# Optimization experiments

Hardware: AMD Instinct MI355X
Metric: run time of the kernel (lower is better)

Reference implementation:

```python
import jax, jax.numpy as jnp
import numpy as np

B, T, IN, CELL, OUT = 512, 32, 512, 128, 128


def setup_inputs() -> dict:
    key = jax.random.key(0)
    ks = jax.random.split(key, 6)
    d = IN + CELL
    w = lambda k, shape, fan: jax.random.normal(k, shape, jnp.float32) / np.sqrt(fan).astype(np.float32)
    return {
        "x": jax.random.normal(ks[0], (B, T, IN), jnp.float32),
        "Wf": w(ks[1], (d, CELL), d), "bf": jnp.zeros((CELL,), jnp.float32),
        "Wi1": w(ks[2], (d, CELL), d), "bi1": jnp.zeros((CELL,), jnp.float32),
        "Wi2": w(ks[3], (d, CELL), d), "bi2": jnp.zeros((CELL,), jnp.float32),
        "Wo": w(ks[4], (d, CELL), d), "bo": jnp.zeros((CELL,), jnp.float32),
        "Wc": w(ks[5], (CELL, OUT), CELL), "bc": jnp.zeros((OUT,), jnp.float32),
    }


def reference(x, Wf, bf, Wi1, bi1, Wi2, bi2, Wo, bo, Wc, bc):
    # Faithful to MyLSTM.forward: loop runs x.shape[1] times; each iteration
    # concatenates the FULL [B,T,CELL] cell_state with the FULL [B,T,IN] x
    # (x is never sliced per step). Only the last iteration's output matters,
    # but we carry it through the scan to match the loop structure exactly.
    Tn = x.shape[1]
    c0 = jnp.zeros(x.shape[:2] + (Wf.shape[1],), x.dtype)
    out0 = jnp.zeros(x.shape[:2] + (Wc.shape[1],), x.dtype)

    def step(carry, _):
        c, _prev_out = carry
        inp = jnp.concatenate([c, x], axis=-1)  # [B,T,CELL+IN]
        f = jax.nn.sigmoid(inp @ Wf + bf)
        c = c * f + jax.nn.sigmoid(inp @ Wi1 + bi1) * jnp.tanh(inp @ Wi2 + bi2)
        o = jax.nn.sigmoid(inp @ Wo + bo) * jnp.tanh(c)
        out = jax.nn.softmax(o @ Wc + bc, axis=2)  # out_features != 1 branch
        return (c, out), None

    (c, out), _ = jax.lax.scan(step, (c0, out0), None, length=Tn)
    return out, c
```

## Files before the change

kernel.cpp:

```cpp
#include <hip/hip_runtime.h>
#include <stdint.h>

#define ROWS  16384
#define CELL  128
#define INF   512
#define RPB   16
#define NSTEP 32

typedef _Float16 f16x8 __attribute__((ext_vector_type(8)));
typedef _Float16 f16x4 __attribute__((ext_vector_type(4)));
typedef float    f32x4 __attribute__((ext_vector_type(4)));

#define MFMA16(a, b, c) __builtin_amdgcn_mfma_f32_16x16x32_f16((a), (b), (c), 0, 0, 0)

#define AOFF  0
#define XOFF  65536
#define WCOFF 327680
#define WSTOT 344064

#define LOG2E  1.44269504f
#define LOG2E2 2.88539008f

__device__ __forceinline__ unsigned short f2h_bits(float f) {
  _Float16 h = (_Float16)f;
  return *(unsigned short*)&h;
}
__device__ __forceinline__ float sig2(float z) {
  return __builtin_amdgcn_rcpf(1.f + __builtin_amdgcn_exp2f(-z));
}
__device__ __forceinline__ float tanh2(float z) {
  return 1.f - 2.f * __builtin_amdgcn_rcpf(__builtin_amdgcn_exp2f(z) + 1.f);
}

__global__ __launch_bounds__(256) void prep_kernel(
    const float* __restrict__ Wf, const float* __restrict__ Wi1,
    const float* __restrict__ Wi2, const float* __restrict__ Wo,
    const float* __restrict__ Wc, unsigned short* __restrict__ ws) {
  int id = blockIdx.x * blockDim.x + threadIdx.x;
  if (id >= WSTOT) return;
  const float* Wg[4] = {Wf, Wi1, Wi2, Wo};
  const float scl[4] = {LOG2E, LOG2E, LOG2E2, LOG2E};
  float v;
  int k, n, base;
  if (id < XOFF) {
    int g = id >> 14, r = id & 16383;
    k = r >> 7; n = r & 127;
    v = Wg[g][k * CELL + n] * scl[g];
    base = g * 16384;
  } else if (id < WCOFF) {
    int t = id - XOFF;
    int g = t >> 16, r = t & 65535;
    k = r >> 7; n = r & 127;
    v = Wg[g][(CELL + k) * CELL + n] * scl[g];
    base = XOFF + g * 65536;
  } else {
    int r = id - WCOFF;
    k = r >> 7; n = r & 127;
    v = Wc[k * CELL + n] * LOG2E;
    base = WCOFF;
  }
  int ks = k >> 5, kk = k & 31;
  int lane = ((kk >> 3) << 4) | (n & 15);
  int j = kk & 7, nb = n >> 4;
  ws[base + ((ks * 8 + nb) * 64 + lane) * 8 + j] = f2h_bits(v);
}

__global__ __launch_bounds__(512, 4) void lstm_kernel(
    const float* __restrict__ x,
    const float* __restrict__ bf_, const float* __restrict__ bi1,
    const float* __restrict__ bi2, const float* __restrict__ bo,
    const float* __restrict__ bc,
    const unsigned short* __restrict__ ws, float* __restrict__ out) {

  __shared__ _Float16 cF[2][16][136];
  __shared__ union {
    _Float16 xs[16][520];
    struct {
      float    e[16][132];
      _Float16 o[16][136];
    } ep;
  } uS;

  const int tid  = threadIdx.x;
  const int lane = tid & 63;
  const int w    = tid >> 6;
  const int n16  = lane & 15;
  const int g4   = lane >> 4;
  const int col0 = w * 16 + g4 * 4;
  const int r0   = blockIdx.x * RPB;

  const _Float16* Aw  = (const _Float16*)ws + AOFF;
  const _Float16* Xw  = (const _Float16*)ws + XOFF;
  const _Float16* Wcw = (const _Float16*)ws + WCOFF;

  const float* xb = x + (size_t)r0 * INF;
  float4 v0a, v0b, v1a, v1b;
  {
    int fa = tid, fb = tid + 512;
    int ra = fa >> 6, ca = fa & 63;
    int rb_ = fb >> 6, cb = fb & 63;
    const float4* pa = (const float4*)(xb + (size_t)ra * INF);
    const float4* pb = (const float4*)(xb + (size_t)rb_ * INF);
    v0a = pa[ca];       v0b = pb[cb];
    v1a = pa[ca + 64];  v1b = pb[cb + 64];
    f16x4 h;
    h = (f16x4){(_Float16)v0a.x, (_Float16)v0a.y, (_Float16)v0a.z, (_Float16)v0a.w};
    *(f16x4*)&uS.xs[ra][ca * 4] = h;
    h = (f16x4){(_Float16)v0b.x, (_Float16)v0b.y, (_Float16)v0b.z, (_Float16)v0b.w};
    *(f16x4*)&uS.xs[rb_][cb * 4] = h;
  }
  __syncthreads();

  f32x4 u[4];
#pragma unroll
  for (int g = 0; g < 4; ++g)
#pragma unroll
    for (int i = 0; i < 4; ++i) u[g][i] = 0.f;

#pragma unroll 4
  for (int ks = 0; ks < 8; ++ks) {
    f16x8 a = *(const f16x8*)&uS.xs[n16][ks * 32 + g4 * 8];
#pragma unroll
    for (int g = 0; g < 4; ++g) {
      f16x8 b = *(const f16x8*)(Xw + g * 65536 + ((ks * 8 + w) * 64 + lane) * 8);
      u[g] = MFMA16(b, a, u[g]);
    }
  }

  {
    int fa = tid, fb = tid + 512;
    int ra = fa >> 6, ca = fa & 63;
    int rb_ = fb >> 6, cb = fb & 63;
    f16x4 h;
    h = (f16x4){(_Float16)v1a.x, (_Float16)v1a.y, (_Float16)v1a.z, (_Float16)v1a.w};
    *(f16x4*)&uS.xs[ra][256 + ca * 4] = h;
    h = (f16x4){(_Float16)v1b.x, (_Float16)v1b.y, (_Float16)v1b.z, (_Float16)v1b.w};
    *(f16x4*)&uS.xs[rb_][256 + cb * 4] = h;
  }
  __syncthreads();

#pragma unroll 4
  for (int ks = 8; ks < 16; ++ks) {
    f16x8 a = *(const f16x8*)&uS.xs[n16][ks * 32 + g4 * 8];
#pragma unroll
    for (int g = 0; g < 4; ++g) {
      f16x8 b = *(const f16x8*)(Xw + g * 65536 + ((ks * 8 + w) * 64 + lane) * 8);
      u[g] = MFMA16(b, a, u[g]);
    }
  }
  {
    f32x4 b0 = *(const f32x4*)&bf_[col0];
    f32x4 b1 = *(const f32x4*)&bi1[col0];
    f32x4 b2 = *(const f32x4*)&bi2[col0];
    f32x4 b3 = *(const f32x4*)&bo[col0];
#pragma unroll
    for (int i = 0; i < 4; ++i) {
      u[0][i] = fmaf(b0[i], LOG2E,  u[0][i]);
      u[1][i] = fmaf(b1[i], LOG2E,  u[1][i]);
      u[2][i] = fmaf(b2[i], LOG2E2, u[2][i]);
      u[3][i] = fmaf(b3[i], LOG2E,  u[3][i]);
    }
  }

  f16x8 wr[3][4];
#pragma unroll
  for (int g = 0; g < 3; ++g)
#pragma unroll
    for (int ks = 0; ks < 4; ++ks)
      wr[g][ks] = *(const f16x8*)(Aw + g * 16384 + ((ks * 8 + w) * 64 + lane) * 8);

  f32x4 cr;
  {
    f16x4 hv;
#pragma unroll
    for (int i = 0; i < 4; ++i) {
      float c0 = sig2(u[1][i]) * tanh2(u[2][i]);
      cr[i] = c0;
      hv[i] = (_Float16)c0;
    }
    *(f16x4*)&cF[0][n16][col0] = hv;
  }
  __syncthreads();

#pragma unroll 1
  for (int t = 1; t < NSTEP - 1; ++t) {
    const _Float16* rd = &cF[(t + 1) & 1][n16][0];
    f16x8 a0 = *(const f16x8*)(rd + g4 * 8);
    f16x8 a1 = *(const f16x8*)(rd + 32 + g4 * 8);
    f16x8 a2 = *(const f16x8*)(rd + 64 + g4 * 8);
    f16x8 a3 = *(const f16x8*)(rd + 96 + g4 * 8);
    __builtin_amdgcn_s_setprio(1);
    f32x4 zf  = MFMA16(wr[0][0], a0, u[0]);
    f32x4 zi1 = MFMA16(wr[1][0], a0, u[1]);
    f32x4 zi2 = MFMA16(wr[2][0], a0, u[2]);
    zf  = MFMA16(wr[0][1], a1, zf);
    zi1 = MFMA16(wr[1][1], a1, zi1);
    zi2 = MFMA16(wr[2][1], a1, zi2);
    zf  = MFMA16(wr[0][2], a2, zf);
    zi1 = MFMA16(wr[1][2], a2, zi1);
    zi2 = MFMA16(wr[2][2], a2, zi2);
    zf  = MFMA16(wr[0][3], a3, zf);
    zi1 = MFMA16(wr[1][3], a3, zi1);
    zi2 = MFMA16(wr[2][3], a3, zi2);
    __builtin_amdgcn_s_setprio(0);
    f16x4 hv;
#pragma unroll
    for (int i = 0; i < 4; ++i) {
      float fg = sig2(zf[i]);
      float ig = sig2(zi1[i]);
      float gg = tanh2(zi2[i]);
      float cn = fmaf(cr[i], fg, ig * gg);
      cr[i] = cn;
      hv[i] = (_Float16)cn;
    }
    *(f16x4*)&cF[t & 1][n16][col0] = hv;
    __syncthreads();
  }

  {
    const _Float16* rd = &cF[0][n16][0];
    f16x8 a0 = *(const f16x8*)(rd + g4 * 8);
    f16x8 a1 = *(const f16x8*)(rd + 32 + g4 * 8);
    f16x8 a2 = *(const f16x8*)(rd + 64 + g4 * 8);
    f16x8 a3 = *(const f16x8*)(rd + 96 + g4 * 8);
    f16x8 bo0 = *(const f16x8*)(Aw + 3 * 16384 + ((0 * 8 + w) * 64 + lane) * 8);
    f16x8 bo1 = *(const f16x8*)(Aw + 3 * 16384 + ((1 * 8 + w) * 64 + lane) * 8);
    f16x8 bo2 = *(const f16x8*)(Aw + 3 * 16384 + ((2 * 8 + w) * 64 + lane) * 8);
    f16x8 bo3 = *(const f16x8*)(Aw + 3 * 16384 + ((3 * 8 + w) * 64 + lane) * 8);
    __builtin_amdgcn_s_setprio(1);
    f32x4 zf  = MFMA16(wr[0][0], a0, u[0]);
    f32x4 zi1 = MFMA16(wr[1][0], a0, u[1]);
    f32x4 zi2 = MFMA16(wr[2][0], a0, u[2]);
    f32x4 zo  = MFMA16(bo0,      a0, u[3]);
    zf  = MFMA16(wr[0][1], a1, zf);
    zi1 = MFMA16(wr[1][1], a1, zi1);
    zi2 = MFMA16(wr[2][1], a1, zi2);
    zo  = MFMA16(bo1,      a1, zo);
    zf  = MFMA16(wr[0][2], a2, zf);
    zi1 = MFMA16(wr[1][2], a2, zi1);
    zi2 = MFMA16(wr[2][2], a2, zi2);
    zo  = MFMA16(bo2,      a2, zo);
    zf  = MFMA16(wr[0][3], a3, zf);
    zi1 = MFMA16(wr[1][3], a3, zi1);
    zi2 = MFMA16(wr[2][3], a3, zi2);
    zo  = MFMA16(bo3,      a3, zo);
    __builtin_amdgcn_s_setprio(0);
    f16x4 hv;
#pragma unroll
    for (int i = 0; i < 4; ++i) {
      float fg = sig2(zf[i]);
      float ig = sig2(zi1[i]);
      float gg = tanh2(zi2[i]);
      float cn = fmaf(cr[i], fg, ig * gg);
      cr[i] = cn;
      float ov = sig2(zo[i]) * tanh2(cn * LOG2E2);
      hv[i] = (_Float16)ov;
    }
    __syncthreads();
    *(f16x4*)&uS.ep.o[n16][col0] = hv;
    __syncthreads();
  }

  {
    f32x4 sacc;
#pragma unroll
    for (int i = 0; i < 4; ++i) sacc[i] = 0.f;
#pragma unroll
    for (int ks = 0; ks < 4; ++ks) {
      f16x8 a = *(const f16x8*)&uS.ep.o[n16][ks * 32 + g4 * 8];
      f16x8 b = *(const f16x8*)(Wcw + ((ks * 8 + w) * 64 + lane) * 8);
      sacc = MFMA16(b, a, sacc);
    }
    f32x4 bcv = *(const f32x4*)&bc[col0];
    f32x4 ev;
#pragma unroll
    for (int i = 0; i < 4; ++i)
      ev[i] = __builtin_amdgcn_exp2f(fmaf(bcv[i], LOG2E, sacc[i]));
    *(f32x4*)&uS.ep.e[n16][col0] = ev;
    __syncthreads();

#pragma unroll
    for (int rr = 0; rr < 2; ++rr) {
      int r = w * 2 + rr;
      float e0 = uS.ep.e[r][lane];
      float e1 = uS.ep.e[r][lane + 64];
      float sm = e0 + e1;
#pragma unroll
      for (int off = 32; off; off >>= 1) sm += __shfl_xor(sm, off, 64);
      float inv = __builtin_amdgcn_rcpf(sm);
      size_t base = (size_t)(r0 + r) * 128;
      out[base + lane]      = e0 * inv;
      out[base + lane + 64] = e1 * inv;
    }

    *(f32x4*)&out[(size_t)ROWS * 128 + (size_t)(r0 + n16) * 128 + col0] = cr;
  }
}

extern "C" void kernel_launch(void* const* d_in, const int* in_sizes, int n_in,
                              void* d_out, int out_size, void* d_ws, size_t ws_size,
                              hipStream_t stream) {
  const float* x   = (const float*)d_in[0];
  const float* Wf  = (const float*)d_in[1];
  const float* bf_ = (const float*)d_in[2];
  const float* Wi1 = (const float*)d_in[3];
  const float* bi1 = (const float*)d_in[4];
  const float* Wi2 = (const float*)d_in[5];
  const float* bi2 = (const float*)d_in[6];
  const float* Wo  = (const float*)d_in[7];
  const float* bo  = (const float*)d_in[8];
  const float* Wc  = (const float*)d_in[9];
  const float* bc  = (const float*)d_in[10];
  unsigned short* ws = (unsigned short*)d_ws;
  float* out = (float*)d_out;

  hipLaunchKernelGGL(prep_kernel, dim3((WSTOT + 255) / 256), dim3(256), 0, stream,
                     Wf, Wi1, Wi2, Wo, Wc, ws);
  hipLaunchKernelGGL(lstm_kernel, dim3(ROWS / RPB), dim3(512), 0, stream,
                     x, bf_, bi1, bi2, bo, bc, ws, out);
}
```

Before: 174.0 us.

## Swizzle LDS tiles with XOR layout, load all x up front, drop setprio

Replaces the padded shared-memory arrays for x, the cell state and the output activations with unpadded buffers that use an XOR swizzle on 16-byte chunks, with the offsets precomputed per lane. The x tile is now loaded and converted in a single pass before one barrier, instead of loading the second half while the first half's MFMAs run. The s_setprio hints around the MFMA chains and one redundant epilogue barrier are removed. The aim is to avoid LDS bank conflicts without padding and to cut barrier overhead, at the cost of losing the overlap of the second x half with compute and the wave-priority hints.

```diff
diff --git a/kernel.cpp b/kernel.cpp
--- a/kernel.cpp
+++ b/kernel.cpp
@@ -72,12 +72,12 @@
     const float* __restrict__ bc,
     const unsigned short* __restrict__ ws, float* __restrict__ out) {
 
-  __shared__ _Float16 cF[2][16][136];
+  __shared__ _Float16 cF[2][16 * 128];
   __shared__ union {
-    _Float16 xs[16][520];
+    _Float16 xs[16 * 512];
     struct {
       float    e[16][132];
-      _Float16 o[16][136];
+      _Float16 o[16 * 128];
     } ep;
   } uS;
 
@@ -86,6 +86,7 @@
   const int w    = tid >> 6;
   const int n16  = lane & 15;
   const int g4   = lane >> 4;
+  const int sxor = n16 & 7;
   const int col0 = w * 16 + g4 * 4;
   const int r0   = blockIdx.x * RPB;
 
@@ -93,21 +94,23 @@
   const _Float16* Xw  = (const _Float16*)ws + XOFF;
   const _Float16* Wcw = (const _Float16*)ws + WCOFF;
 
-  const float* xb = x + (size_t)r0 * INF;
-  float4 v0a, v0b, v1a, v1b;
-  {
-    int fa = tid, fb = tid + 512;
-    int ra = fa >> 6, ca = fa & 63;
-    int rb_ = fb >> 6, cb = fb & 63;
-    const float4* pa = (const float4*)(xb + (size_t)ra * INF);
-    const float4* pb = (const float4*)(xb + (size_t)rb_ * INF);
-    v0a = pa[ca];       v0b = pb[cb];
-    v1a = pa[ca + 64];  v1b = pb[cb + 64];
-    f16x4 h;
-    h = (f16x4){(_Float16)v0a.x, (_Float16)v0a.y, (_Float16)v0a.z, (_Float16)v0a.w};
-    *(f16x4*)&uS.xs[ra][ca * 4] = h;
-    h = (f16x4){(_Float16)v0b.x, (_Float16)v0b.y, (_Float16)v0b.z, (_Float16)v0b.w};
-    *(f16x4*)&uS.xs[rb_][cb * 4] = h;
+  int aoff[4];
+#pragma unroll
+  for (int ks = 0; ks < 4; ++ks)
+    aoff[ks] = n16 * 128 + (((4 * ks + g4) ^ sxor) << 3);
+  const int woff = n16 * 128 + (((2 * w + (g4 >> 1)) ^ sxor) << 3) + (g4 & 1) * 4;
+
+  {
+    const float* xb = x + (size_t)r0 * INF;
+#pragma unroll
+    for (int i = 0; i < 4; ++i) {
+      int flat = tid + i * 512;
+      int row = flat >> 7, c4 = flat & 127;
+      const float4 v = ((const float4*)(xb + (size_t)row * INF))[c4];
+      f16x4 h = {(_Float16)v.x, (_Float16)v.y, (_Float16)v.z, (_Float16)v.w};
+      int idx = row * 512 + (((c4 >> 1) ^ (row & 7)) << 3) + (c4 & 1) * 4;
+      *(f16x4*)&uS.xs[idx] = h;
+    }
   }
   __syncthreads();
 
@@ -118,30 +121,8 @@
     for (int i = 0; i < 4; ++i) u[g][i] = 0.f;
 
 #pragma unroll 4
-  for (int ks = 0; ks < 8; ++ks) {
-    f16x8 a = *(const f16x8*)&uS.xs[n16][ks * 32 + g4 * 8];
-#pragma unroll
-    for (int g = 0; g < 4; ++g) {
-      f16x8 b = *(const f16x8*)(Xw + g * 65536 + ((ks * 8 + w) * 64 + lane) * 8);
-      u[g] = MFMA16(b, a, u[g]);
-    }
-  }
-
-  {
-    int fa = tid, fb = tid + 512;
-    int ra = fa >> 6, ca = fa & 63;
-    int rb_ = fb >> 6, cb = fb & 63;
-    f16x4 h;
-    h = (f16x4){(_Float16)v1a.x, (_Float16)v1a.y, (_Float16)v1a.z, (_Float16)v1a.w};
-    *(f16x4*)&uS.xs[ra][256 + ca * 4] = h;
-    h = (f16x4){(_Float16)v1b.x, (_Float16)v1b.y, (_Float16)v1b.z, (_Float16)v1b.w};
-    *(f16x4*)&uS.xs[rb_][256 + cb * 4] = h;
-  }
-  __syncthreads();
-
-#pragma unroll 4
-  for (int ks = 8; ks < 16; ++ks) {
-    f16x8 a = *(const f16x8*)&uS.xs[n16][ks * 32 + g4 * 8];
+  for (int ks = 0; ks < 16; ++ks) {
+    f16x8 a = *(const f16x8*)&uS.xs[n16 * 512 + (((4 * ks + g4) ^ sxor) << 3)];
 #pragma unroll
     for (int g = 0; g < 4; ++g) {
       f16x8 b = *(const f16x8*)(Xw + g * 65536 + ((ks * 8 + w) * 64 + lane) * 8);
@@ -178,18 +159,17 @@
       cr[i] = c0;
       hv[i] = (_Float16)c0;
     }
-    *(f16x4*)&cF[0][n16][col0] = hv;
+    *(f16x4*)&cF[0][woff] = hv;
   }
   __syncthreads();
 
 #pragma unroll 1
   for (int t = 1; t < NSTEP - 1; ++t) {
-    const _Float16* rd = &cF[(t + 1) & 1][n16][0];
-    f16x8 a0 = *(const f16x8*)(rd + g4 * 8);
-    f16x8 a1 = *(const f16x8*)(rd + 32 + g4 * 8);
-    f16x8 a2 = *(const f16x8*)(rd + 64 + g4 * 8);
-    f16x8 a3 = *(const f16x8*)(rd + 96 + g4 * 8);
-    __builtin_amdgcn_s_setprio(1);
+    const _Float16* rd = cF[(t + 1) & 1];
+    f16x8 a0 = *(const f16x8*)(rd + aoff[0]);
+    f16x8 a1 = *(const f16x8*)(rd + aoff[1]);
+    f16x8 a2 = *(const f16x8*)(rd + aoff[2]);
+    f16x8 a3 = *(const f16x8*)(rd + aoff[3]);
     f32x4 zf  = MFMA16(wr[0][0], a0, u[0]);
     f32x4 zi1 = MFMA16(wr[1][0], a0, u[1]);
     f32x4 zi2 = MFMA16(wr[2][0], a0, u[2]);
@@ -202,7 +182,6 @@
     zf  = MFMA16(wr[0][3], a3, zf);
     zi1 = MFMA16(wr[1][3], a3, zi1);
     zi2 = MFMA16(wr[2][3], a3, zi2);
-    __builtin_amdgcn_s_setprio(0);
     f16x4 hv;
 #pragma unroll
     for (int i = 0; i < 4; ++i) {
@@ -213,21 +192,20 @@
       cr[i] = cn;
       hv[i] = (_Float16)cn;
     }
-    *(f16x4*)&cF[t & 1][n16][col0] = hv;
+    *(f16x4*)&cF[t & 1][woff] = hv;
     __syncthreads();
   }
 
   {
-    const _Float16* rd = &cF[0][n16][0];
-    f16x8 a0 = *(const f16x8*)(rd + g4 * 8);
-    f16x8 a1 = *(const f16x8*)(rd + 32 + g4 * 8);
-    f16x8 a2 = *(const f16x8*)(rd + 64 + g4 * 8);
-    f16x8 a3 = *(const f16x8*)(rd + 96 + g4 * 8);
+    const _Float16* rd = cF[0];
+    f16x8 a0 = *(const f16x8*)(rd + aoff[0]);
+    f16x8 a1 = *(const f16x8*)(rd + aoff[1]);
+    f16x8 a2 = *(const f16x8*)(rd + aoff[2]);
+    f16x8 a3 = *(const f16x8*)(rd + aoff[3]);
     f16x8 bo0 = *(const f16x8*)(Aw + 3 * 16384 + ((0 * 8 + w) * 64 + lane) * 8);
     f16x8 bo1 = *(const f16x8*)(Aw + 3 * 16384 + ((1 * 8 + w) * 64 + lane) * 8);
     f16x8 bo2 = *(const f16x8*)(Aw + 3 * 16384 + ((2 * 8 + w) * 64 + lane) * 8);
     f16x8 bo3 = *(const f16x8*)(Aw + 3 * 16384 + ((3 * 8 + w) * 64 + lane) * 8);
-    __builtin_amdgcn_s_setprio(1);
     f32x4 zf  = MFMA16(wr[0][0], a0, u[0]);
     f32x4 zi1 = MFMA16(wr[1][0], a0, u[1]);
     f32x4 zi2 = MFMA16(wr[2][0], a0, u[2]);
@@ -244,7 +222,6 @@
     zi1 = MFMA16(wr[1][3], a3, zi1);
     zi2 = MFMA16(wr[2][3], a3, zi2);
     zo  = MFMA16(bo3,      a3, zo);
-    __builtin_amdgcn_s_setprio(0);
     f16x4 hv;
 #pragma unroll
     for (int i = 0; i < 4; ++i) {
@@ -256,9 +233,8 @@
       float ov = sig2(zo[i]) * tanh2(cn * LOG2E2);
       hv[i] = (_Float16)ov;
     }
+    *(f16x4*)&uS.ep.o[woff] = hv;
     __syncthreads();
-    *(f16x4*)&uS.ep.o[n16][col0] = hv;
-    __syncthreads();
   }
 
   {
@@ -267,7 +243,7 @@
     for (int i = 0; i < 4; ++i) sacc[i] = 0.f;
 #pragma unroll
     for (int ks = 0; ks < 4; ++ks) {
-      f16x8 a = *(const f16x8*)&uS.ep.o[n16][ks * 32 + g4 * 8];
+      f16x8 a = *(const f16x8*)&uS.ep.o[aoff[ks]];
       f16x8 b = *(const f16x8*)(Wcw + ((ks * 8 + w) * 64 + lane) * 8);
       sacc = MFMA16(b, a, sacc);
     }
```

Result: faster. 167.8 us (-3.6%).
